# Performance work log

Hardware: AMD Instinct MI355X
Metric: run time of the kernel (lower is better)

The kernel has to match this reference:

```python
import jax, jax.numpy as jnp
import numpy as np

N_Q = 32      # questions per batch
N_DOCS = 8    # docs per question (positive first)
Q_LEN = 32    # query tokens
D_LEN = 200   # doc tokens
DIM = 128     # ColBERT embedding dim


def setup_inputs() -> dict:
    key = jax.random.key(0)
    k1, k2 = jax.random.split(key)
    hq = jax.random.normal(k1, (N_Q, Q_LEN, DIM), dtype=jnp.float32)
    hd = jax.random.normal(k2, (N_Q * N_DOCS, D_LEN, DIM), dtype=jnp.float32)
    return {"hq": hq, "hd": hd}


def reference(hq, hd):
    # ColBERT maxsim: [n, m, q, d] token-level scores
    scores = jnp.einsum("nqh,mdh->nmqd", hq, hd)
    # max over doc tokens, mean over query tokens -> [n, m]
    score_matrix = jnp.max(scores, axis=-1).mean(axis=-1)

    n, m = score_matrix.shape
    n_docs = m // n
    # positive doc is the first in each group: targets = [0, n_docs, 2*n_docs, ...]
    targets = jnp.arange(0, m, n_docs)
    logp = jax.nn.log_softmax(score_matrix, axis=-1)
    loss = -jnp.mean(jnp.take_along_axis(logp, targets[:, None], axis=1))
    return score_matrix, loss
```

## Files before the change

### kernel.cpp

```cpp
#include <hip/hip_runtime.h>
#include <hip/hip_bf16.h>
#include <math.h>

typedef short short8 __attribute__((ext_vector_type(8)));
typedef float f32x4 __attribute__((ext_vector_type(4)));

#define NQ 32
#define NDOCS 8
#define QLEN 32
#define DLEN 200
#define DIM 128
#define MD 256
#define HD_ROWS 208
#define DOC_SHORTS (HD_ROWS * DIM)
#define DOC_BYTES (DOC_SHORTS * 2)
#define DOC_CHUNKS (HD_ROWS * 16)

__device__ __forceinline__ short f2bf(float x) {
    union { float f; unsigned u; } v; v.f = x;
    unsigned r = v.u + 0x7FFFu + ((v.u >> 16) & 1u);
    return (short)(r >> 16);
}

__device__ __forceinline__ short8 cvt8(float4 f0, float4 f1) {
    short8 o;
    o[0] = f2bf(f0.x); o[1] = f2bf(f0.y); o[2] = f2bf(f0.z); o[3] = f2bf(f0.w);
    o[4] = f2bf(f1.x); o[5] = f2bf(f1.y); o[6] = f2bf(f1.z); o[7] = f2bf(f1.w);
    return o;
}

__global__ __launch_bounds__(256) void convert_hd(const float* __restrict__ hd,
                                                  short* __restrict__ hdb) {
    unsigned c = blockIdx.x * 256 + threadIdx.x;
    unsigned m = c / DOC_CHUNKS;
    unsigned rc = c - m * DOC_CHUNKS;
    unsigned row = rc >> 4, kc = rc & 15;
    short8 o = {0, 0, 0, 0, 0, 0, 0, 0};
    if (row < DLEN) {
        const float4* p = reinterpret_cast<const float4*>(
            hd + ((size_t)m * DLEN + row) * DIM + kc * 8);
        o = cvt8(p[0], p[1]);
    }
    unsigned dst = m * DOC_CHUNKS + row * 16 + (kc ^ (row & 7));
    reinterpret_cast<short8*>(hdb)[dst] = o;
}

__global__ __launch_bounds__(256) void colbert_scores(const float* __restrict__ hq,
                                                      const short* __restrict__ hdb,
                                                      float* __restrict__ out) {
    __shared__ char lds[DOC_BYTES];
    const int tid = threadIdx.x;
    const int b = blockIdx.x;
    const int m = b & 255, qg = b >> 8;
    const int wid = tid >> 6, lane = tid & 63;
    const int lg = lane >> 4, lr = lane & 15;
    const int n = qg * 4 + wid;

    const char* gsrc = reinterpret_cast<const char*>(hdb + (size_t)m * DOC_SHORTS);
    {
        const int gbase = wid * 1024 + lane * 16;
        #pragma unroll
        for (int i = 0; i < 13; ++i)
            __builtin_amdgcn_global_load_lds(
                (const __attribute__((address_space(1))) void*)(gsrc + i * 4096 + gbase),
                (__attribute__((address_space(3))) void*)(lds + i * 4096 + wid * 1024),
                16, 0, 0);
    }

    short8 Bq[2][4];
    #pragma unroll
    for (int qt = 0; qt < 2; ++qt)
        #pragma unroll
        for (int s = 0; s < 4; ++s) {
            const float4* p = reinterpret_cast<const float4*>(
                hq + (size_t)(n * QLEN + qt * 16 + lr) * DIM + s * 32 + lg * 8);
            Bq[qt][s] = cvt8(p[0], p[1]);
        }

    __syncthreads();

    int va[4];
    #pragma unroll
    for (int s = 0; s < 4; ++s)
        va[s] = lr * 256 + ((s * 64 + lg * 16) ^ ((lr & 7) << 4));

    float qmax0 = -INFINITY, qmax1 = -INFINITY;

#define STEP(DT, MASKED)                                                          \
    {                                                                             \
        f32x4 a0 = {0.f, 0.f, 0.f, 0.f}, a1 = {0.f, 0.f, 0.f, 0.f};               \
        _Pragma("unroll")                                                         \
        for (int s = 0; s < 4; ++s) {                                             \
            short8 A_ = *reinterpret_cast<const short8*>(&lds[va[s] + (DT) * 4096]); \
            a0 = __builtin_amdgcn_mfma_f32_16x16x32_bf16(A_, Bq[0][s], a0, 0, 0, 0); \
            a1 = __builtin_amdgcn_mfma_f32_16x16x32_bf16(A_, Bq[1][s], a1, 0, 0, 0); \
        }                                                                         \
        if (!(MASKED) || lg < 2) {                                                \
            qmax0 = fmaxf(qmax0, fmaxf(fmaxf(a0[0], a0[1]), fmaxf(a0[2], a0[3])));\
            qmax1 = fmaxf(qmax1, fmaxf(fmaxf(a1[0], a1[1]), fmaxf(a1[2], a1[3])));\
        }                                                                         \
    }

    #pragma unroll
    for (int dt = 0; dt < 12; ++dt) STEP(dt, false);
    STEP(12, true);
#undef STEP

    #pragma unroll
    for (int off = 16; off <= 32; off <<= 1) {
        qmax0 = fmaxf(qmax0, __shfl_xor(qmax0, off, 64));
        qmax1 = fmaxf(qmax1, __shfl_xor(qmax1, off, 64));
    }
    float s = qmax0 + qmax1;
    #pragma unroll
    for (int off = 1; off <= 8; off <<= 1) s += __shfl_xor(s, off, 64);
    if (lane == 0) out[(size_t)n * MD + m] = s * (1.0f / 32.0f);
}

__global__ __launch_bounds__(256) void colbert_loss(const float* __restrict__ scores,
                                                    float* __restrict__ loss_out) {
    __shared__ float terms[NQ];
    const int tid = threadIdx.x;
    const int wid = tid >> 6, lane = tid & 63;
    for (int n = wid; n < NQ; n += 4) {
        const float* row = scores + n * MD;
        float v0 = row[lane], v1 = row[64 + lane], v2 = row[128 + lane], v3 = row[192 + lane];
        float mx = fmaxf(fmaxf(v0, v1), fmaxf(v2, v3));
        #pragma unroll
        for (int off = 1; off < 64; off <<= 1) mx = fmaxf(mx, __shfl_xor(mx, off, 64));
        float s = expf(v0 - mx) + expf(v1 - mx) + expf(v2 - mx) + expf(v3 - mx);
        #pragma unroll
        for (int off = 1; off < 64; off <<= 1) s += __shfl_xor(s, off, 64);
        if (lane == 0) terms[n] = (mx + logf(s)) - row[n * NDOCS];
    }
    __syncthreads();
    if (tid == 0) {
        float acc = 0.f;
        #pragma unroll
        for (int n = 0; n < NQ; ++n) acc += terms[n];
        loss_out[0] = acc * (1.0f / NQ);
    }
}

extern "C" void kernel_launch(void* const* d_in, const int* in_sizes, int n_in,
                              void* d_out, int out_size, void* d_ws, size_t ws_size,
                              hipStream_t stream) {
    const float* hq = (const float*)d_in[0];
    const float* hd = (const float*)d_in[1];
    float* out = (float*)d_out;
    short* hdb = (short*)d_ws;

    convert_hd<<<3328, 256, 0, stream>>>(hd, hdb);
    colbert_scores<<<2048, 256, 0, stream>>>(hq, hdb, out);
    colbert_loss<<<1, 256, 0, stream>>>(out, out + NQ * MD);
}
```

Before: 40.90 us.

## Fuse bf16 conversion into scoring kernel with one block per document

Removes the separate fp32-to-bf16 conversion pass and its workspace round trip. The scoring kernel now loads each document's fp32 embeddings once, converts them into swizzled LDS, and has 16 waves each score 2 questions against that doc. This cuts global traffic and one launch, but loses the async global-to-LDS load and limits the grid to 256 large blocks, with conversion latency exposed per block.

After: 96.17 us. 135% more time.

```diff
diff --git a/kernel.cpp b/kernel.cpp
--- a/kernel.cpp
+++ b/kernel.cpp
@@ -11,10 +11,8 @@
 #define DLEN 200
 #define DIM 128
 #define MD 256
-#define HD_ROWS 208
-#define DOC_SHORTS (HD_ROWS * DIM)
-#define DOC_BYTES (DOC_SHORTS * 2)
-#define DOC_CHUNKS (HD_ROWS * 16)
+#define DOC_FLOATS (DLEN * DIM)
+#define ROWB 256
 
 __device__ __forceinline__ short f2bf(float x) {
     union { float f; unsigned u; } v; v.f = x;
@@ -29,62 +27,57 @@
     return o;
 }
 
-__global__ __launch_bounds__(256) void convert_hd(const float* __restrict__ hd,
-                                                  short* __restrict__ hdb) {
-    unsigned c = blockIdx.x * 256 + threadIdx.x;
-    unsigned m = c / DOC_CHUNKS;
-    unsigned rc = c - m * DOC_CHUNKS;
-    unsigned row = rc >> 4, kc = rc & 15;
-    short8 o = {0, 0, 0, 0, 0, 0, 0, 0};
-    if (row < DLEN) {
-        const float4* p = reinterpret_cast<const float4*>(
-            hd + ((size_t)m * DLEN + row) * DIM + kc * 8);
-        o = cvt8(p[0], p[1]);
-    }
-    unsigned dst = m * DOC_CHUNKS + row * 16 + (kc ^ (row & 7));
-    reinterpret_cast<short8*>(hdb)[dst] = o;
+__device__ __forceinline__ void writeChunk(char* lds, int c, float4 f0, float4 f1) {
+    int row = c >> 4, kc = c & 15;
+    int byte = row * ROWB + ((kc * 16) ^ ((row & 7) << 4));
+    *reinterpret_cast<short8*>(&lds[byte]) = cvt8(f0, f1);
 }
 
-__global__ __launch_bounds__(256) void colbert_scores(const float* __restrict__ hq,
-                                                      const short* __restrict__ hdb,
+__global__ __launch_bounds__(1024) void colbert_fused(const float* __restrict__ hq,
+                                                      const float* __restrict__ hd,
                                                       float* __restrict__ out) {
-    __shared__ char lds[DOC_BYTES];
+    __shared__ char lds[208 * ROWB];
+    const int m = blockIdx.x;
     const int tid = threadIdx.x;
-    const int b = blockIdx.x;
-    const int m = b & 255, qg = b >> 8;
     const int wid = tid >> 6, lane = tid & 63;
     const int lg = lane >> 4, lr = lane & 15;
-    const int n = qg * 4 + wid;
 
-    const char* gsrc = reinterpret_cast<const char*>(hdb + (size_t)m * DOC_SHORTS);
-    {
-        const int gbase = wid * 1024 + lane * 16;
-        #pragma unroll
-        for (int i = 0; i < 13; ++i)
-            __builtin_amdgcn_global_load_lds(
-                (const __attribute__((address_space(1))) void*)(gsrc + i * 4096 + gbase),
-                (__attribute__((address_space(3))) void*)(lds + i * 4096 + wid * 1024),
-                16, 0, 0);
+    const float4* src4 = reinterpret_cast<const float4*>(hd + (size_t)m * DOC_FLOATS);
+    #pragma unroll
+    for (int k = 0; k < 3; ++k) {
+        int c = tid + k * 1024;
+        float4 f0 = src4[c * 2], f1 = src4[c * 2 + 1];
+        writeChunk(lds, c, f0, f1);
     }
-
-    short8 Bq[2][4];
-    #pragma unroll
-    for (int qt = 0; qt < 2; ++qt)
-        #pragma unroll
-        for (int s = 0; s < 4; ++s) {
-            const float4* p = reinterpret_cast<const float4*>(
-                hq + (size_t)(n * QLEN + qt * 16 + lr) * DIM + s * 32 + lg * 8);
-            Bq[qt][s] = cvt8(p[0], p[1]);
-        }
-
+    if (tid < 128) {
+        int c = 3072 + tid;
+        float4 f0 = src4[c * 2], f1 = src4[c * 2 + 1];
+        writeChunk(lds, c, f0, f1);
+        float4 z = {0.f, 0.f, 0.f, 0.f};
+        writeChunk(lds, 3200 + tid, z, z);
+    }
     __syncthreads();
 
     int va[4];
     #pragma unroll
     for (int s = 0; s < 4; ++s)
-        va[s] = lr * 256 + ((s * 64 + lg * 16) ^ ((lr & 7) << 4));
+        va[s] = lr * ROWB + ((s * 64 + lg * 16) ^ ((lr & 7) << 4));
 
-    float qmax0 = -INFINITY, qmax1 = -INFINITY;
+    #pragma unroll 1
+    for (int qi = 0; qi < 2; ++qi) {
+        const int n = wid * 2 + qi;
+
+        short8 Bq[2][4];
+        #pragma unroll
+        for (int qt = 0; qt < 2; ++qt)
+            #pragma unroll
+            for (int s = 0; s < 4; ++s) {
+                const float4* p = reinterpret_cast<const float4*>(
+                    hq + (size_t)(n * QLEN + qt * 16 + lr) * DIM + s * 32 + lg * 8);
+                Bq[qt][s] = cvt8(p[0], p[1]);
+            }
+
+        float qmax0 = -INFINITY, qmax1 = -INFINITY;
 
 #define STEP(DT, MASKED)                                                          \
     {                                                                             \
@@ -101,20 +94,21 @@
         }                                                                         \
     }
 
-    #pragma unroll
-    for (int dt = 0; dt < 12; ++dt) STEP(dt, false);
-    STEP(12, true);
+        #pragma unroll
+        for (int dt = 0; dt < 12; ++dt) STEP(dt, false);
+        STEP(12, true);
 #undef STEP
 
-    #pragma unroll
-    for (int off = 16; off <= 32; off <<= 1) {
-        qmax0 = fmaxf(qmax0, __shfl_xor(qmax0, off, 64));
-        qmax1 = fmaxf(qmax1, __shfl_xor(qmax1, off, 64));
+        #pragma unroll
+        for (int off = 16; off <= 32; off <<= 1) {
+            qmax0 = fmaxf(qmax0, __shfl_xor(qmax0, off, 64));
+            qmax1 = fmaxf(qmax1, __shfl_xor(qmax1, off, 64));
+        }
+        float s = qmax0 + qmax1;
+        #pragma unroll
+        for (int off = 1; off <= 8; off <<= 1) s += __shfl_xor(s, off, 64);
+        if (lane == 0) out[(size_t)n * MD + m] = s * (1.0f / 32.0f);
     }
-    float s = qmax0 + qmax1;
-    #pragma unroll
-    for (int off = 1; off <= 8; off <<= 1) s += __shfl_xor(s, off, 64);
-    if (lane == 0) out[(size_t)n * MD + m] = s * (1.0f / 32.0f);
 }
 
 __global__ __launch_bounds__(256) void colbert_loss(const float* __restrict__ scores,
@@ -148,9 +142,7 @@
     const float* hq = (const float*)d_in[0];
     const float* hd = (const float*)d_in[1];
     float* out = (float*)d_out;
-    short* hdb = (short*)d_ws;
 
-    convert_hd<<<3328, 256, 0, stream>>>(hd, hdb);
-    colbert_scores<<<2048, 256, 0, stream>>>(hq, hdb, out);
+    colbert_fused<<<MD, 1024, 0, stream>>>(hq, hd, out);
     colbert_loss<<<1, 256, 0, stream>>>(out, out + NQ * MD);
 }
```

## Pipeline doc tile loads with compute stages and remap conversion blocks per XCD

Applied to the files above, without the earlier changes.

The scores kernel now issues the async global-to-LDS doc loads after the query conversion. Instead of one full barrier, it waits on partial vmcnt counts so the MFMA steps on the first doc tiles can start while later tiles are still in flight. The conversion kernel's block-to-doc mapping is interleaved so that doc m is produced by a block with the same index modulo 8 as the scores blocks that consume it. This aims to keep converted data in the same XCD's L2. The cost is extra barriers and hand-tuned waitcnt values that depend on the exact ordering of memory operations.

After: 41.64 us. Within noise of the previous version (+1.8%).

```diff
diff --git a/kernel.cpp b/kernel.cpp
--- a/kernel.cpp
+++ b/kernel.cpp
@@ -31,9 +31,12 @@
 
 __global__ __launch_bounds__(256) void convert_hd(const float* __restrict__ hd,
                                                   short* __restrict__ hdb) {
-    unsigned c = blockIdx.x * 256 + threadIdx.x;
-    unsigned m = c / DOC_CHUNKS;
-    unsigned rc = c - m * DOC_CHUNKS;
+    const unsigned b = blockIdx.x;
+    const unsigned x = b & 7, g = b >> 3;
+    unsigned idx = g * 256 + threadIdx.x;
+    unsigned dc = idx / DOC_CHUNKS;
+    unsigned rc = idx - dc * DOC_CHUNKS;
+    unsigned m = dc * 8 + x;
     unsigned row = rc >> 4, kc = rc & 15;
     short8 o = {0, 0, 0, 0, 0, 0, 0, 0};
     if (row < DLEN) {
@@ -56,17 +59,6 @@
     const int lg = lane >> 4, lr = lane & 15;
     const int n = qg * 4 + wid;
 
-    const char* gsrc = reinterpret_cast<const char*>(hdb + (size_t)m * DOC_SHORTS);
-    {
-        const int gbase = wid * 1024 + lane * 16;
-        #pragma unroll
-        for (int i = 0; i < 13; ++i)
-            __builtin_amdgcn_global_load_lds(
-                (const __attribute__((address_space(1))) void*)(gsrc + i * 4096 + gbase),
-                (__attribute__((address_space(3))) void*)(lds + i * 4096 + wid * 1024),
-                16, 0, 0);
-    }
-
     short8 Bq[2][4];
     #pragma unroll
     for (int qt = 0; qt < 2; ++qt)
@@ -77,7 +69,26 @@
             Bq[qt][s] = cvt8(p[0], p[1]);
         }
 
-    __syncthreads();
+    const char* gsrc = reinterpret_cast<const char*>(hdb) + (size_t)m * DOC_BYTES;
+    const int goff = wid * 1024 + lane * 16;
+    const int lbase = wid * 1024;
+    #pragma unroll
+    for (int i = 0; i < 8; ++i)
+        __builtin_amdgcn_global_load_lds(
+            (const __attribute__((address_space(1))) void*)(gsrc + i * 4096 + goff),
+            (__attribute__((address_space(3))) void*)(lds + i * 4096 + lbase),
+            16, 0, 0);
+
+    asm volatile("s_waitcnt vmcnt(4)" ::: "memory");
+    __builtin_amdgcn_s_barrier();
+    __builtin_amdgcn_sched_barrier(0);
+
+    #pragma unroll
+    for (int i = 8; i < 13; ++i)
+        __builtin_amdgcn_global_load_lds(
+            (const __attribute__((address_space(1))) void*)(gsrc + i * 4096 + goff),
+            (__attribute__((address_space(3))) void*)(lds + i * 4096 + lbase),
+            16, 0, 0);
 
     int va[4];
     #pragma unroll
@@ -102,7 +113,21 @@
     }
 
     #pragma unroll
-    for (int dt = 0; dt < 12; ++dt) STEP(dt, false);
+    for (int dt = 0; dt < 4; ++dt) STEP(dt, false);
+
+    asm volatile("s_waitcnt vmcnt(5)" ::: "memory");
+    __builtin_amdgcn_s_barrier();
+    __builtin_amdgcn_sched_barrier(0);
+
+    #pragma unroll
+    for (int dt = 4; dt < 8; ++dt) STEP(dt, false);
+
+    asm volatile("s_waitcnt vmcnt(0)" ::: "memory");
+    __builtin_amdgcn_s_barrier();
+    __builtin_amdgcn_sched_barrier(0);
+
+    #pragma unroll
+    for (int dt = 8; dt < 12; ++dt) STEP(dt, false);
     STEP(12, true);
 #undef STEP
 
```
